# Kernel optimization log

Hardware: AMD Instinct MI355X
Metric: run time of the kernel (lower is better)

Reference implementation:

```python
import jax, jax.numpy as jnp
import numpy as np
import math

HIDDEN = 1024
N_HEADS = 16
HEAD_DIM = HIDDEN // N_HEADS  # 64
B, S = 4, 8192


def setup_inputs() -> dict:
    key = jax.random.key(0)
    ks = jax.random.split(key, 5)
    scale = 1.0 / math.sqrt(HIDDEN)
    return {
        "hidden_states": jax.random.normal(ks[0], (B, S, HIDDEN), dtype=jnp.float32),
        "Wq": jax.random.normal(ks[1], (HIDDEN, HIDDEN), dtype=jnp.float32) * scale,
        "Wk": jax.random.normal(ks[2], (HIDDEN, HIDDEN), dtype=jnp.float32) * scale,
        "Wv": jax.random.normal(ks[3], (HIDDEN, HIDDEN), dtype=jnp.float32) * scale,
        "Wo": jax.random.normal(ks[4], (HIDDEN, HIDDEN), dtype=jnp.float32) * scale,
    }


def reference(hidden_states, Wq, Wk, Wv, Wo):
    b, s, _ = hidden_states.shape
    # nn.Linear(bias=False): y = x @ W.T
    q = (hidden_states @ Wq.T).reshape(b, s, N_HEADS, HEAD_DIM)
    k = (hidden_states @ Wk.T).reshape(b, s, N_HEADS, HEAD_DIM)
    v = (hidden_states @ Wv.T).reshape(b, s, N_HEADS, HEAD_DIM)
    # Faithful to source: NO transpose to (b,h,s,d); matmul contracts head_dim
    # per (batch, position), yielding [b, s, h, h] head-mixing weights.
    attn = jnp.einsum("bshd,bstd->bsht", q, k) / math.sqrt(HEAD_DIM)
    attn = jax.nn.softmax(attn, axis=-1)
    out = jnp.einsum("bsht,bstd->bshd", attn, v).reshape(b, s, HIDDEN)
    return out @ Wo.T
```

## Files before the change

kernel.cpp:

```cpp
#include <hip/hip_runtime.h>
#include <hip/hip_bf16.h>


typedef short bf16x8 __attribute__((ext_vector_type(8)));
typedef float f32x4  __attribute__((ext_vector_type(4)));

__device__ __forceinline__ float bf2f(short u) {
    union { unsigned int ui; float f; } cv;
    cv.ui = ((unsigned int)(unsigned short)u) << 16;
    return cv.f;
}
__device__ __forceinline__ short f2bf(float f) {
    __hip_bfloat16 h = __float2bfloat16(f);
    return *reinterpret_cast<short*>(&h);
}

__device__ __forceinline__ void gload_lds16(const void* g, void* lds) {
    const unsigned __attribute__((address_space(1)))* gp =
        reinterpret_cast<const unsigned __attribute__((address_space(1)))*>((unsigned long long)g);
    unsigned __attribute__((address_space(3)))* lp =
        reinterpret_cast<unsigned __attribute__((address_space(3)))*>(
            (unsigned int)(unsigned long long)lds);
    __builtin_amdgcn_global_load_lds(gp, lp, 16, 0, 0);
}

__global__ void detect_dtype(const unsigned* __restrict__ x, int* __restrict__ flag) {
    __shared__ int cnt;
    if (threadIdx.x == 0) cnt = 0;
    __syncthreads();
    int c = 0;
    for (int i = threadIdx.x; i < 4096; i += 256) {
        const unsigned u = x[(long)i * 4001 + 3];
        const unsigned b = (u >> 7) & 0xFF;
        c += (b >= 0x70 && b <= 0x87) ? 1 : 0;
    }
    atomicAdd(&cnt, c);
    __syncthreads();
    if (threadIdx.x == 0) *flag = (cnt > 2048) ? 0 : 1;
}

__global__ void convert_all(const void* __restrict__ X,
                            const void* __restrict__ W0, const void* __restrict__ W1,
                            const void* __restrict__ W2, const void* __restrict__ W3,
                            short* __restrict__ dst, long total,
                            const int* __restrict__ flag) {
    constexpr long WELEM = 1024 * 1024;
    const int f = *flag;
    const long step = (long)gridDim.x * blockDim.x * 8;
    for (long i = ((long)blockIdx.x * blockDim.x + threadIdx.x) * 8; i < total; i += step) {
        const void* src;
        long off;
        if (i < 4 * WELEM) {
            const int w = (int)(i >> 20);
            src = (w == 0) ? W0 : (w == 1) ? W1 : (w == 2) ? W2 : W3;
            off = i & (WELEM - 1);
        } else {
            src = X;
            off = i - 4 * WELEM;
        }
        if (f) {
            const float* s = (const float*)src + off;
            const f32x4 a = *(const f32x4*)s;
            const f32x4 b = *(const f32x4*)(s + 4);
            bf16x8 o;
            o[0] = f2bf(a[0]); o[1] = f2bf(a[1]); o[2] = f2bf(a[2]); o[3] = f2bf(a[3]);
            o[4] = f2bf(b[0]); o[5] = f2bf(b[1]); o[6] = f2bf(b[2]); o[7] = f2bf(b[3]);
            *(bf16x8*)(dst + i) = o;
        } else {
            *(bf16x8*)(dst + i) = *(const bf16x8*)((const short*)src + off);
        }
    }
}

__device__ __forceinline__ void gemm256_core(const short* __restrict__ A,
                                             const short* __restrict__ W,
                                             void* __restrict__ C,
                                             const int* flag_fp32,
                                             long m0, int n0, short* lds) {
    constexpr int K = 1024, N = 1024;
    const int tid  = threadIdx.x;
    const int lane = tid & 63;
    const int wid  = tid >> 6;
    const int wm = wid >> 1, wn = wid & 1;

    short* A0 = lds;
    short* B0 = lds + 16384;
    short* A1 = lds + 32768;
    short* B1 = lds + 49152;

    const int srl = tid >> 3;
    const int kcs = (tid & 7) ^ (srl & 7);
    int aoff[8], boff[8];
    #pragma unroll
    for (int i = 0; i < 8; ++i) {
        const int row = i * 32 + srl;
        aoff[i] = (int)((m0 + row) * K + kcs * 8);
        boff[i] = (n0 + row) * K + kcs * 8;
    }
    const int ldsw = wid * 512;

    f32x4 acc[8][8] = {};

    #pragma unroll
    for (int i = 0; i < 8; ++i) gload_lds16(A + aoff[i], A0 + i * 2048 + ldsw);
    #pragma unroll
    for (int i = 0; i < 8; ++i) gload_lds16(W + boff[i], B0 + i * 2048 + ldsw);
    asm volatile("s_waitcnt vmcnt(0)" ::: "memory");
    __builtin_amdgcn_s_barrier();

    const int arow = wm * 128 + (lane & 15);
    const int brow = wn * 128 + (lane & 15);

    for (int t = 0; t < 16; ++t) {
        const int cur = t & 1;
        const short* rA = cur ? A1 : A0;
        const short* rB = cur ? B1 : B0;
        short* sA = cur ? A0 : A1;
        short* sB = cur ? B0 : B1;
        const int kadd = (t + 1) * 64;
        const bool more = (t < 15);

        #pragma unroll
        for (int ks = 0; ks < 2; ++ks) {
            const int kx8 = ((ks * 4 + (lane >> 4)) ^ (lane & 7)) * 8;
            bf16x8 af[8], bfr[8];
            #pragma unroll
            for (int m = 0; m < 8; ++m)
                af[m] = *(const bf16x8*)(rA + ((arow + m * 16) * 64) + kx8);
            #pragma unroll
            for (int n = 0; n < 8; ++n)
                bfr[n] = *(const bf16x8*)(rB + ((brow + n * 16) * 64) + kx8);
            __builtin_amdgcn_sched_barrier(0);
            __builtin_amdgcn_s_barrier();
            __builtin_amdgcn_sched_barrier(0);
            if (more) {
                if (ks == 0) {
                    #pragma unroll
                    for (int i = 0; i < 8; ++i)
                        gload_lds16(A + aoff[i] + kadd, sA + i * 2048 + ldsw);
                } else {
                    #pragma unroll
                    for (int i = 0; i < 8; ++i)
                        gload_lds16(W + boff[i] + kadd, sB + i * 2048 + ldsw);
                }
            }
            asm volatile("s_waitcnt lgkmcnt(0)" ::: "memory");
            __builtin_amdgcn_sched_barrier(0);
            __builtin_amdgcn_s_setprio(1);
            #pragma unroll
            for (int m = 0; m < 8; ++m)
                #pragma unroll
                for (int n = 0; n < 8; ++n)
                    acc[m][n] = __builtin_amdgcn_mfma_f32_16x16x32_bf16(
                                    af[m], bfr[n], acc[m][n], 0, 0, 0);
            __builtin_amdgcn_s_setprio(0);
            __builtin_amdgcn_sched_barrier(0);
            if (ks == 1) {
                asm volatile("s_waitcnt vmcnt(0)" ::: "memory");
                __builtin_amdgcn_s_barrier();
            }
        }
    }

    const int f = flag_fp32 ? *flag_fp32 : 0;
    #pragma unroll
    for (int mf = 0; mf < 8; ++mf) {
        #pragma unroll
        for (int nf = 0; nf < 8; ++nf) {
            const int  col   = n0 + wn * 128 + nf * 16 + (lane & 15);
            const long rbase = m0 + wm * 128 + mf * 16 + (lane >> 4) * 4;
            if (f) {
                float* Cf = (float*)C;
                #pragma unroll
                for (int r = 0; r < 4; ++r)
                    Cf[(rbase + r) * N + col] = acc[mf][nf][r];
            } else {
                short* Cs = (short*)C;
                #pragma unroll
                for (int r = 0; r < 4; ++r)
                    Cs[(rbase + r) * N + col] = f2bf(acc[mf][nf][r]);
            }
        }
    }
}

__global__ __launch_bounds__(256, 1) void gemm_qkv256(const short* __restrict__ A,
                                                      const short* __restrict__ W0,
                                                      const short* __restrict__ W1,
                                                      const short* __restrict__ W2,
                                                      short* __restrict__ C0,
                                                      short* __restrict__ C1,
                                                      short* __restrict__ C2) {
    __shared__ __align__(16) short lds[65536];
    const int nwg = gridDim.x;
    const int q8  = nwg >> 3;
    const int d   = blockIdx.x;
    const int lin = (d & 7) * q8 + (d >> 3);
    const int x   = lin / 12;
    const int r   = lin - x * 12;
    const int yy  = r / 3;
    const int z   = r - yy * 3;
    const short* W = (z == 0) ? W0 : (z == 1) ? W1 : W2;
    short*       C = (z == 0) ? C0 : (z == 1) ? C1 : C2;
    gemm256_core(A, W, C, nullptr, (long)x * 256, yy * 256, lds);
}

__global__ __launch_bounds__(256, 1) void gemm_out256(const short* __restrict__ A,
                                                      const short* __restrict__ W,
                                                      void* __restrict__ C,
                                                      long moff,
                                                      const int* __restrict__ flag) {
    __shared__ __align__(16) short lds[65536];
    const int nwg = gridDim.x;
    const int q8  = nwg >> 3;
    const int d   = blockIdx.x;
    const int lin = (d & 7) * q8 + (d >> 3);
    const int x   = lin >> 2;
    const int yy  = lin & 3;
    gemm256_core(A, W, C, flag, moff + (long)x * 256, yy * 256, lds);
}

__global__ __launch_bounds__(256) void attn_mix(const short* __restrict__ Q,
                                                const short* __restrict__ K,
                                                const short* __restrict__ V,
                                                short* __restrict__ Z) {
    constexpr int RS = 72;
    __shared__ short sq[4][16 * RS];
    __shared__ short sk[4][16 * RS];
    __shared__ short sv[4][16 * RS];
    __shared__ float sp[4][256];

    const int  tid  = threadIdx.x;
    const int  lane = tid & 63;
    const int  w    = tid >> 6;
    const long tok  = (long)blockIdx.x * 4 + w;

    const short* qg = Q + tok * 1024;
    const short* kg = K + tok * 1024;
    const short* vg = V + tok * 1024;

    #pragma unroll
    for (int it = 0; it < 2; ++it) {
        const int c   = lane + 64 * it;
        const int row = c >> 3;
        const int cc  = (c & 7) * 8;
        *(bf16x8*)&sq[w][row * RS + cc] = *(const bf16x8*)(qg + c * 8);
        *(bf16x8*)&sk[w][row * RS + cc] = *(const bf16x8*)(kg + c * 8);
        *(bf16x8*)&sv[w][row * RS + cc] = *(const bf16x8*)(vg + c * 8);
    }
    __syncthreads();

    const int h  = lane >> 2;
    const int t0 = (lane & 3) * 4;
    float sc[4] = {0.f, 0.f, 0.f, 0.f};
    for (int d = 0; d < 64; ++d) {
        const float qv = bf2f(sq[w][h * RS + d]);
        #pragma unroll
        for (int j = 0; j < 4; ++j)
            sc[j] += qv * bf2f(sk[w][(t0 + j) * RS + d]);
    }
    #pragma unroll
    for (int j = 0; j < 4; ++j) sc[j] *= 0.125f;

    float mx = fmaxf(fmaxf(sc[0], sc[1]), fmaxf(sc[2], sc[3]));
    mx = fmaxf(mx, __shfl_xor(mx, 1));
    mx = fmaxf(mx, __shfl_xor(mx, 2));
    float ex[4], s = 0.f;
    #pragma unroll
    for (int j = 0; j < 4; ++j) { ex[j] = __expf(sc[j] - mx); s += ex[j]; }
    s += __shfl_xor(s, 1);
    s += __shfl_xor(s, 2);
    const float inv = 1.f / s;
    #pragma unroll
    for (int j = 0; j < 4; ++j) sp[w][h * 16 + t0 + j] = ex[j] * inv;
    __syncthreads();

    const int dbase = (lane & 3) * 16;
    float o[16] = {};
    for (int t = 0; t < 16; ++t) {
        const float p = sp[w][h * 16 + t];
        const bf16x8 v0 = *(const bf16x8*)&sv[w][t * RS + dbase];
        const bf16x8 v1 = *(const bf16x8*)&sv[w][t * RS + dbase + 8];
        #pragma unroll
        for (int e = 0; e < 8; ++e) {
            o[e]     += p * bf2f(v0[e]);
            o[e + 8] += p * bf2f(v1[e]);
        }
    }
    bf16x8 ov0, ov1;
    #pragma unroll
    for (int e = 0; e < 8; ++e) { ov0[e] = f2bf(o[e]); ov1[e] = f2bf(o[e + 8]); }
    *(bf16x8*)(Z + tok * 1024 + lane * 16)     = ov0;
    *(bf16x8*)(Z + tok * 1024 + lane * 16 + 8) = ov1;
}

extern "C" void kernel_launch(void* const* d_in, const int* in_sizes, int n_in,
                              void* d_out, int out_size, void* d_ws, size_t ws_size,
                              hipStream_t stream) {
    const void* X = d_in[0];

    const long TOT = 32768;
    constexpr long WELEM = 1024 * 1024;

    char* ws   = (char*)d_ws;
    int*  flag = (int*)ws;
    short* Wqb = (short*)(ws + 256);
    short* Wkb = Wqb + WELEM;
    short* Wvb = Wkb + WELEM;
    short* Wob = Wvb + WELEM;
    short* dyn = Wob + WELEM;

    const size_t fixed = 256 + 4 * WELEM * 2;
    long chunk = 256;
    const long tiers[4] = {32768, 8192, 2048, 512};
    for (int i = 0; i < 4; ++i)
        if (fixed + (size_t)6 * tiers[i] * 1024 * 2 <= ws_size) { chunk = tiers[i]; break; }

    short* Xb = dyn;
    short* Qb = Xb + chunk * 1024;
    short* Kb = Qb + chunk * 1024;
    short* Vb = Kb + chunk * 1024;
    short* Zb = Vb + chunk * 1024;

    detect_dtype<<<1, 256, 0, stream>>>((const unsigned*)X, flag);

    if (chunk == TOT) {
        convert_all<<<2048, 256, 0, stream>>>(X, d_in[1], d_in[2], d_in[3], d_in[4],
                                              Wqb, 4 * WELEM + TOT * 1024, flag);
        gemm_qkv256<<<dim3((TOT / 256) * 12), 256, 0, stream>>>(Xb, Wqb, Wkb, Wvb,
                                                                Qb, Kb, Vb);
        attn_mix<<<dim3(TOT / 4), 256, 0, stream>>>(Qb, Kb, Vb, Zb);
        gemm_out256<<<dim3((TOT / 256) * 4), 256, 0, stream>>>(Zb, Wob, d_out, 0, flag);
    } else {
        convert_all<<<512, 256, 0, stream>>>(X, d_in[1], d_in[2], d_in[3], d_in[4],
                                             Wqb, 4 * WELEM, flag);
        for (long t0 = 0; t0 < TOT; t0 += chunk) {
            convert_all<<<2048, 256, 0, stream>>>(
                (const void*)((const char*)X + (size_t)t0 * 1024 * 4),
                d_in[1], d_in[2], d_in[3], d_in[4],
                Xb - 4 * WELEM, 4 * WELEM + chunk * 1024, flag);
            gemm_qkv256<<<dim3((chunk / 256) * 12), 256, 0, stream>>>(Xb, Wqb, Wkb, Wvb,
                                                                      Qb, Kb, Vb);
            attn_mix<<<dim3(chunk / 4), 256, 0, stream>>>(Qb, Kb, Vb, Zb);
            gemm_out256<<<dim3((chunk / 256) * 4), 256, 0, stream>>>(Zb - t0 * 1024, Wob,
                                                                     d_out, t0, flag);
        }
    }
}
```

Measured before the change: 404.5 us.

## Use 8-wave 512-thread workgroups for QKV projection GEMM

Adds a new GEMM core for the QKV projection in which eight waves share the 256x256 tile, each computing a 128x64 subtile instead of 128x128. The workgroup grows from 256 to 512 threads and launch bounds allow two workgroups per CU. Each thread also issues half as many global-to-LDS loads per stage. The aim is more waves per CU and smaller per-wave accumulator sets, to hide memory and LDS latency better. The cost is more fragment reloads of A from LDS per wave, and tighter register and LDS limits may keep the second workgroup per CU from fitting, since each workgroup uses 128KB of LDS.

```diff
diff --git a/kernel.cpp b/kernel.cpp
--- a/kernel.cpp
+++ b/kernel.cpp
@@ -72,11 +72,120 @@
     }
 }
 
-__device__ __forceinline__ void gemm256_core(const short* __restrict__ A,
-                                             const short* __restrict__ W,
-                                             void* __restrict__ C,
-                                             const int* flag_fp32,
-                                             long m0, int n0, short* lds) {
+__device__ __forceinline__ void gemm256_core8(const short* __restrict__ A,
+                                              const short* __restrict__ W,
+                                              void* __restrict__ C,
+                                              const int* flag_fp32,
+                                              long m0, int n0, short* lds) {
+    constexpr int K = 1024, N = 1024;
+    const int tid  = threadIdx.x;
+    const int lane = tid & 63;
+    const int wid  = tid >> 6;
+    const int wm = wid >> 2, wn = wid & 3;
+
+    short* A0 = lds;
+    short* B0 = lds + 16384;
+    short* A1 = lds + 32768;
+    short* B1 = lds + 49152;
+
+    const int srl = tid >> 3;
+    const int kcs = (tid & 7) ^ (srl & 7);
+    int aoff[4], boff[4];
+    #pragma unroll
+    for (int i = 0; i < 4; ++i) {
+        const int row = i * 64 + srl;
+        aoff[i] = (int)((m0 + row) * K + kcs * 8);
+        boff[i] = (n0 + row) * K + kcs * 8;
+    }
+    const int ldsw = wid * 512;
+
+    f32x4 acc[8][4] = {};
+
+    #pragma unroll
+    for (int i = 0; i < 4; ++i) gload_lds16(A + aoff[i], A0 + i * 4096 + ldsw);
+    #pragma unroll
+    for (int i = 0; i < 4; ++i) gload_lds16(W + boff[i], B0 + i * 4096 + ldsw);
+    asm volatile("s_waitcnt vmcnt(0)" ::: "memory");
+    __builtin_amdgcn_s_barrier();
+
+    for (int t = 0; t < 16; ++t) {
+        const int cur = t & 1;
+        const short* rA = cur ? A1 : A0;
+        const short* rB = cur ? B1 : B0;
+        short* sA = cur ? A0 : A1;
+        short* sB = cur ? B0 : B1;
+        const int kadd = (t + 1) * 64;
+        const bool more = (t < 15);
+
+        #pragma unroll
+        for (int ks = 0; ks < 2; ++ks) {
+            const int kx8 = ((ks * 4 + (lane >> 4)) ^ (lane & 7)) * 8;
+            bf16x8 af[8], bfr[4];
+            #pragma unroll
+            for (int m = 0; m < 8; ++m)
+                af[m] = *(const bf16x8*)(rA + ((wm * 128 + m * 16 + (lane & 15)) * 64) + kx8);
+            #pragma unroll
+            for (int n = 0; n < 4; ++n)
+                bfr[n] = *(const bf16x8*)(rB + ((wn * 64 + n * 16 + (lane & 15)) * 64) + kx8);
+            __builtin_amdgcn_sched_barrier(0);
+            __builtin_amdgcn_s_barrier();
+            __builtin_amdgcn_sched_barrier(0);
+            if (more) {
+                if (ks == 0) {
+                    #pragma unroll
+                    for (int i = 0; i < 4; ++i)
+                        gload_lds16(A + aoff[i] + kadd, sA + i * 4096 + ldsw);
+                } else {
+                    #pragma unroll
+                    for (int i = 0; i < 4; ++i)
+                        gload_lds16(W + boff[i] + kadd, sB + i * 4096 + ldsw);
+                }
+            }
+            asm volatile("s_waitcnt lgkmcnt(0)" ::: "memory");
+            __builtin_amdgcn_sched_barrier(0);
+            __builtin_amdgcn_s_setprio(1);
+            #pragma unroll
+            for (int m = 0; m < 8; ++m)
+                #pragma unroll
+                for (int n = 0; n < 4; ++n)
+                    acc[m][n] = __builtin_amdgcn_mfma_f32_16x16x32_bf16(
+                                    af[m], bfr[n], acc[m][n], 0, 0, 0);
+            __builtin_amdgcn_s_setprio(0);
+            __builtin_amdgcn_sched_barrier(0);
+            if (ks == 1) {
+                asm volatile("s_waitcnt vmcnt(0)" ::: "memory");
+                __builtin_amdgcn_s_barrier();
+            }
+        }
+    }
+
+    const int f = flag_fp32 ? *flag_fp32 : 0;
+    #pragma unroll
+    for (int mf = 0; mf < 8; ++mf) {
+        #pragma unroll
+        for (int nf = 0; nf < 4; ++nf) {
+            const int  col   = n0 + wn * 64 + nf * 16 + (lane & 15);
+            const long rbase = m0 + wm * 128 + mf * 16 + (lane >> 4) * 4;
+            if (f) {
+                float* Cf = (float*)C;
+                #pragma unroll
+                for (int r = 0; r < 4; ++r)
+                    Cf[(rbase + r) * N + col] = acc[mf][nf][r];
+            } else {
+                short* Cs = (short*)C;
+                #pragma unroll
+                for (int r = 0; r < 4; ++r)
+                    Cs[(rbase + r) * N + col] = f2bf(acc[mf][nf][r]);
+            }
+        }
+    }
+}
+
+__device__ __forceinline__ void gemm256_core4(const short* __restrict__ A,
+                                              const short* __restrict__ W,
+                                              void* __restrict__ C,
+                                              const int* flag_fp32,
+                                              long m0, int n0, short* lds) {
     constexpr int K = 1024, N = 1024;
     const int tid  = threadIdx.x;
     const int lane = tid & 63;
@@ -184,7 +293,7 @@
     }
 }
 
-__global__ __launch_bounds__(256, 1) void gemm_qkv256(const short* __restrict__ A,
+__global__ __launch_bounds__(512, 2) void gemm_qkv256(const short* __restrict__ A,
                                                       const short* __restrict__ W0,
                                                       const short* __restrict__ W1,
                                                       const short* __restrict__ W2,
@@ -202,7 +311,7 @@
     const int z   = r - yy * 3;
     const short* W = (z == 0) ? W0 : (z == 1) ? W1 : W2;
     short*       C = (z == 0) ? C0 : (z == 1) ? C1 : C2;
-    gemm256_core(A, W, C, nullptr, (long)x * 256, yy * 256, lds);
+    gemm256_core8(A, W, C, nullptr, (long)x * 256, yy * 256, lds);
 }
 
 __global__ __launch_bounds__(256, 1) void gemm_out256(const short* __restrict__ A,
@@ -217,7 +326,7 @@
     const int lin = (d & 7) * q8 + (d >> 3);
     const int x   = lin >> 2;
     const int yy  = lin & 3;
-    gemm256_core(A, W, C, flag, moff + (long)x * 256, yy * 256, lds);
+    gemm256_core4(A, W, C, flag, moff + (long)x * 256, yy * 256, lds);
 }
 
 __global__ __launch_bounds__(256) void attn_mix(const short* __restrict__ Q,
@@ -327,7 +436,7 @@
     if (chunk == TOT) {
         convert_all<<<2048, 256, 0, stream>>>(X, d_in[1], d_in[2], d_in[3], d_in[4],
                                               Wqb, 4 * WELEM + TOT * 1024, flag);
-        gemm_qkv256<<<dim3((TOT / 256) * 12), 256, 0, stream>>>(Xb, Wqb, Wkb, Wvb,
+        gemm_qkv256<<<dim3((TOT / 256) * 12), 512, 0, stream>>>(Xb, Wqb, Wkb, Wvb,
                                                                 Qb, Kb, Vb);
         attn_mix<<<dim3(TOT / 4), 256, 0, stream>>>(Qb, Kb, Vb, Zb);
         gemm_out256<<<dim3((TOT / 256) * 4), 256, 0, stream>>>(Zb, Wob, d_out, 0, flag);
@@ -339,7 +448,7 @@
                 (const void*)((const char*)X + (size_t)t0 * 1024 * 4),
                 d_in[1], d_in[2], d_in[3], d_in[4],
                 Xb - 4 * WELEM, 4 * WELEM + chunk * 1024, flag);
-            gemm_qkv256<<<dim3((chunk / 256) * 12), 256, 0, stream>>>(Xb, Wqb, Wkb, Wvb,
+            gemm_qkv256<<<dim3((chunk / 256) * 12), 512, 0, stream>>>(Xb, Wqb, Wkb, Wvb,
                                                                       Qb, Kb, Vb);
             attn_mix<<<dim3(chunk / 4), 256, 0, stream>>>(Qb, Kb, Vb, Zb);
             gemm_out256<<<dim3((chunk / 256) * 4), 256, 0, stream>>>(Zb - t0 * 1024, Wob,
```

Result: no change. 405.8 us (+0.3%).
